# Optimization experiments

Measured on AMD Instinct MI355X. Metric: run time of the kernel, lower is better.

## Reference

```python
import jax, jax.numpy as jnp
import numpy as np

B, S, D = 2, 2048, 1024
HEADS, HEAD_DIM = 16, 64

def setup_inputs() -> dict:
    key = jax.random.key(0)
    ks = jax.random.split(key, 5)
    sc = 0.02
    return {
        "hidden_states": jax.random.normal(ks[0], (B, S, D), jnp.float32),
        "Wq": jax.random.normal(ks[1], (D, HEADS * HEAD_DIM), jnp.float32) * sc,
        "Wk": jax.random.normal(ks[2], (D, HEADS * HEAD_DIM), jnp.float32) * sc,
        "Wv": jax.random.normal(ks[3], (D, HEADS * HEAD_DIM), jnp.float32) * sc,
        "Wo": jax.random.normal(ks[4], (HEADS * HEAD_DIM, D), jnp.float32) * sc,
        "bo": jnp.zeros((D,), jnp.float32),
    }

def reference(hidden_states, Wq, Wk, Wv, Wo, bo):
    b, s, _ = hidden_states.shape
    # QKV projections (no bias, as in diffusers Attention defaults)
    q = (hidden_states @ Wq).reshape(b, s, HEADS, HEAD_DIM).transpose(0, 2, 1, 3)
    k = (hidden_states @ Wk).reshape(b, s, HEADS, HEAD_DIM).transpose(0, 2, 1, 3)
    v = (hidden_states @ Wv).reshape(b, s, HEADS, HEAD_DIM).transpose(0, 2, 1, 3)
    scale = 1.0 / jnp.sqrt(jnp.asarray(HEAD_DIM, hidden_states.dtype))
    scores = jnp.einsum('bhqd,bhkd->bhqk', q, k) * scale  # full NxN scores
    attn = jax.nn.softmax(scores, axis=-1)
    out = jnp.einsum('bhqk,bhkd->bhqd', attn, v)
    out = out.transpose(0, 2, 1, 3).reshape(b, s, HEADS * HEAD_DIM)
    return out @ Wo + bo
```

## Files before the change

kernel.cpp:

```cpp
#include <hip/hip_runtime.h>

#define B_ 2
#define S_ 2048
#define D_ 1024
#define H_ 16
#define HD_ 64
#define M_ (B_ * S_)

typedef __attribute__((ext_vector_type(4))) float f32x4;
typedef __attribute__((ext_vector_type(16))) float f32x16;
typedef __attribute__((ext_vector_type(8))) short s16x8;
typedef unsigned short u16;
typedef unsigned int u32;

#define QSCALE 0.1803368801111204f

__device__ __forceinline__ u16 f2bf(float f) {
  unsigned u = __float_as_uint(f);
  u += 0x7fffu + ((u >> 16) & 1u);
  return (u16)(u >> 16);
}

__device__ __forceinline__ u32 cvtpk_bf16(float lo, float hi) {
  u32 r;
  asm("v_cvt_pk_bf16_f32 %0, %1, %2" : "=v"(r) : "v"(lo), "v"(hi));
  return r;
}

__device__ __forceinline__ void g2lds16(const u16* g, u16* l) {
  __builtin_amdgcn_global_load_lds((const __attribute__((address_space(1))) u32*)(g),
                                   (__attribute__((address_space(3))) u32*)(l), 16, 0, 0);
}

__global__ __launch_bounds__(256) void prep_kernel(
    const float* __restrict__ X, const float* __restrict__ Wq,
    const float* __restrict__ Wk, const float* __restrict__ Wv,
    const float* __restrict__ Wo, u16* __restrict__ Xb, u16* __restrict__ Wt0) {
  __shared__ float tile[32][33];
  const int id = blockIdx.x;
  if (id < 4096) {
    int i = (id * 256 + threadIdx.x) * 4;
    const float4 v = *(const float4*)(X + i);
    ushort4 o;
    o.x = f2bf(v.x); o.y = f2bf(v.y); o.z = f2bf(v.z); o.w = f2bf(v.w);
    *(ushort4*)(Xb + i) = o;
    return;
  }
  const int id2 = id - 4096;
  const int z = id2 >> 10;
  const float* W = (z == 0) ? Wq : (z == 1) ? Wk : (z == 2) ? Wv : Wo;
  u16* Wt = Wt0 + (size_t)z * (D_ * D_);
  const float sc = (z == 0) ? QSCALE : 1.0f;
  const int tx = threadIdx.x & 31, ty = threadIdx.x >> 5;
  const int c0 = (id2 & 31) * 32, r0 = ((id2 >> 5) & 31) * 32;
#pragma unroll
  for (int j = 0; j < 32; j += 8)
    tile[ty + j][tx] = W[(size_t)(r0 + ty + j) * D_ + c0 + tx];
  __syncthreads();
#pragma unroll
  for (int j = 0; j < 32; j += 8)
    Wt[(size_t)(c0 + ty + j) * D_ + r0 + tx] = f2bf(tile[tx][ty + j] * sc);
}

__global__ __launch_bounds__(256) void gemm_qkv_kernel(
    const u16* __restrict__ Xb, const u16* __restrict__ WqT,
    const u16* __restrict__ WkT, const u16* __restrict__ WvT,
    u16* __restrict__ Qb, u16* __restrict__ Kb, u16* __restrict__ Vt) {
  __shared__ u16 As[2][128 * 32];
  __shared__ u16 Bs[2][128 * 32];
  const int tid = threadIdx.x;
  const int lane = tid & 63, wid = tid >> 6;
  const int wr = wid >> 1, wc = wid & 1;
  const int l15 = lane & 15, l4 = lane >> 4;
  const int bm = blockIdx.x * 128;
  const int bn128 = blockIdx.y;
  const int sel = bn128 >> 3;
  const u16* Wt = (sel == 0) ? WqT : (sel == 1) ? WkT : WvT;
  const int bn = (bn128 & 7) * 128;
  const int r0 = lane >> 2;
  const int c0 = lane & 3;

#define GSTAGE(buf, kt)                                                          \
  do {                                                                           \
    _Pragma("unroll") for (int j = 0; j < 2; ++j) {                              \
      const int row = (wid * 2 + j) * 16 + r0;                                   \
      g2lds16(Xb + (size_t)(bm + row) * D_ + (kt) + c0 * 8,                      \
              &As[buf][(wid * 2 + j) * 512]);                                    \
      g2lds16(Wt + (size_t)(bn + row) * D_ + (kt) + c0 * 8,                      \
              &Bs[buf][(wid * 2 + j) * 512]);                                    \
    }                                                                            \
  } while (0)

  f32x4 acc[4][4] = {};
  GSTAGE(0, 0);
  __syncthreads();
  int cur = 0;
  for (int kt = 0; kt < D_; kt += 32) {
    GSTAGE(cur ^ 1, (kt + 32) & (D_ - 1));
    s16x8 af[4], bfr[4];
#pragma unroll
    for (int i = 0; i < 4; ++i) af[i] = *(const s16x8*)&As[cur][(wr * 64 + i * 16 + l15) * 32 + l4 * 8];
#pragma unroll
    for (int j = 0; j < 4; ++j) bfr[j] = *(const s16x8*)&Bs[cur][(wc * 64 + j * 16 + l15) * 32 + l4 * 8];
#pragma unroll
    for (int i = 0; i < 4; ++i)
#pragma unroll
      for (int j = 0; j < 4; ++j)
        acc[i][j] = __builtin_amdgcn_mfma_f32_16x16x32_bf16(af[i], bfr[j], acc[i][j], 0, 0, 0);
    __syncthreads();
    cur ^= 1;
  }
#undef GSTAGE
#pragma unroll
  for (int i = 0; i < 4; ++i)
#pragma unroll
    for (int j = 0; j < 4; ++j)
#pragma unroll
      for (int r = 0; r < 4; ++r) {
        int m = bm + wr * 64 + i * 16 + l4 * 4 + r;
        int n = bn + wc * 64 + j * 16 + l15;
        int bb = m >> 11, s = m & (S_ - 1);
        int h = n >> 6, d = n & 63;
        u16 v = f2bf(acc[i][j][r]);
        size_t bhsel = (size_t)bb * H_ + h;
        if (sel == 0)      Qb[(bhsel * S_ + s) * HD_ + d] = v;
        else if (sel == 1) Kb[(bhsel * S_ + s) * HD_ + d] = v;
        else               Vt[(bhsel * HD_ + d) * S_ + s] = v;
      }
}

__global__ __launch_bounds__(512, 4) void attn_kernel(
    const u16* __restrict__ Qb, const u16* __restrict__ Kb,
    const u16* __restrict__ Vt, u16* __restrict__ Ob) {
  __shared__ char smem_raw[65536];
  typedef u16 (*lds_t)[2][4096];
  lds_t Ks = (lds_t)smem_raw;
  lds_t Vs = (lds_t)(smem_raw + 32768);
  const int tid = threadIdx.x;
  const int lane = tid & 63, wid = tid >> 6;
  const int qg = wid & 3, half = wid >> 2;
  const int l31 = lane & 31, hi = lane >> 5;
  const int id = blockIdx.x;
  const int bh = (id & 7) * 4 + ((id >> 3) >> 4);
  const int qx = (id >> 3) & 15;
  const size_t kbase = (size_t)bh * S_ * HD_;
  const size_t vbase = (size_t)bh * HD_ * S_;
  const int q0 = qx * 128 + qg * 32;
  const int r0 = lane >> 3;
  const int cs = ((lane & 7) ^ r0) * 8;
  const int kv0 = half << 10;

#define STAGE(buf, kvv)                                                          \
  do {                                                                           \
    _Pragma("unroll") for (int j = 0; j < 2; ++j) {                              \
      const int row = (qg * 2 + j) * 8 + r0;                                     \
      g2lds16(Kb + kbase + (size_t)((kvv) + row) * HD_ + cs,                     \
              &Ks[half][buf][(qg * 2 + j) * 512]);                               \
      g2lds16(Vt + vbase + (size_t)row * S_ + (kvv) + cs,                        \
              &Vs[half][buf][(qg * 2 + j) * 512]);                               \
    }                                                                            \
  } while (0)

  STAGE(0, kv0);

  s16x8 aq[4];
#pragma unroll
  for (int kc = 0; kc < 4; ++kc)
    aq[kc] = *(const s16x8*)(Qb + kbase + (size_t)(q0 + l31) * HD_ + kc * 16 + hi * 8);

  const short one_bf = (short)0x3F80;
  const s16x8 ones8 = {one_bf, one_bf, one_bf, one_bf, one_bf, one_bf, one_bf, one_bf};

  f32x16 acc0 = {}, acc1 = {}, lsacc = {};

  int choff[4];
#pragma unroll
  for (int c = 0; c < 4; ++c) choff[c] = ((c * 2 + hi) ^ (l31 & 7)) * 8;

  __syncthreads();

  for (int t = 0; t < 16; ++t) {
    const int buf = t & 1;
    STAGE(buf ^ 1, kv0 + (((t + 1) & 15) << 6));

    f32x16 s0 = {}, s1 = {};
    __builtin_amdgcn_s_setprio(1);
#pragma unroll
    for (int kc = 0; kc < 4; ++kc) {
      const s16x8 ka0 = *(const s16x8*)&Ks[half][buf][(l31) * 64 + choff[kc]];
      const s16x8 ka1 = *(const s16x8*)&Ks[half][buf][(32 + l31) * 64 + choff[kc]];
      s0 = __builtin_amdgcn_mfma_f32_32x32x16_bf16(ka0, aq[kc], s0, 0, 0, 0);
      s1 = __builtin_amdgcn_mfma_f32_32x32x16_bf16(ka1, aq[kc], s1, 0, 0, 0);
    }
    __builtin_amdgcn_s_setprio(0);

#pragma unroll
    for (int r = 0; r < 16; ++r) {
      s0[r] = __builtin_amdgcn_exp2f(s0[r]);
      s1[r] = __builtin_amdgcn_exp2f(s1[r]);
    }

    s16x8 pa[4];
#pragma unroll
    for (int c = 0; c < 4; ++c) {
      const int rr = (c & 1) * 8;
      u32 a0, a1, b0, b1;
      if (c < 2) {
        a0 = cvtpk_bf16(s0[rr + 0], s0[rr + 1]);
        a1 = cvtpk_bf16(s0[rr + 2], s0[rr + 3]);
        b0 = cvtpk_bf16(s0[rr + 4], s0[rr + 5]);
        b1 = cvtpk_bf16(s0[rr + 6], s0[rr + 7]);
      } else {
        a0 = cvtpk_bf16(s1[rr + 0], s1[rr + 1]);
        a1 = cvtpk_bf16(s1[rr + 2], s1[rr + 3]);
        b0 = cvtpk_bf16(s1[rr + 4], s1[rr + 5]);
        b1 = cvtpk_bf16(s1[rr + 6], s1[rr + 7]);
      }
      asm volatile("v_permlane32_swap_b32 %0, %1" : "+v"(a0), "+v"(b0));
      asm volatile("v_permlane32_swap_b32 %0, %1" : "+v"(a1), "+v"(b1));
      union { u32 u[4]; s16x8 v; } pk;
      pk.u[0] = a0; pk.u[1] = a1; pk.u[2] = b0; pk.u[3] = b1;
      pa[c] = pk.v;
    }

    __builtin_amdgcn_s_setprio(1);
#pragma unroll
    for (int c = 0; c < 4; ++c) {
      const s16x8 vb0 = *(const s16x8*)&Vs[half][buf][(l31) * 64 + choff[c]];
      const s16x8 vb1 = *(const s16x8*)&Vs[half][buf][(32 + l31) * 64 + choff[c]];
      acc0 = __builtin_amdgcn_mfma_f32_32x32x16_bf16(pa[c], vb0, acc0, 0, 0, 0);
      acc1 = __builtin_amdgcn_mfma_f32_32x32x16_bf16(pa[c], vb1, acc1, 0, 0, 0);
      lsacc = __builtin_amdgcn_mfma_f32_32x32x16_bf16(pa[c], ones8, lsacc, 0, 0, 0);
    }
    __builtin_amdgcn_s_setprio(0);

    __syncthreads();
  }
#undef STAGE

  float (*MB)[64][49] = (float(*)[64][49])smem_raw;
  if (half) {
#pragma unroll
    for (int r = 0; r < 16; ++r) {
      MB[qg][lane][r] = acc0[r];
      MB[qg][lane][16 + r] = acc1[r];
      MB[qg][lane][32 + r] = lsacc[r];
    }
  }
  __syncthreads();
  if (!half) {
    const int bb = bh >> 4, h = bh & 15;
#pragma unroll
    for (int r = 0; r < 16; ++r) {
      const float o0 = acc0[r] + MB[qg][lane][r];
      const float o1 = acc1[r] + MB[qg][lane][16 + r];
      const float rinv = 1.0f / (lsacc[r] + MB[qg][lane][32 + r]);
      const int qrow = (r & 3) + 8 * (r >> 2) + 4 * hi;
      const int q = q0 + qrow;
      Ob[(size_t)(bb * S_ + q) * (H_ * HD_) + h * HD_ + l31] = f2bf(o0 * rinv);
      Ob[(size_t)(bb * S_ + q) * (H_ * HD_) + h * HD_ + 32 + l31] = f2bf(o1 * rinv);
    }
  }
}

__global__ __launch_bounds__(256, 2) void gemm_o_kernel(
    const u16* __restrict__ A, const u16* __restrict__ Bt,
    const float* __restrict__ bias, float* __restrict__ C) {
  __shared__ u16 As[2][128 * 32];
  __shared__ u16 Bs[2][64 * 32];
  const int tid = threadIdx.x;
  const int lane = tid & 63, wid = tid >> 6;
  const int l15 = lane & 15, l4 = lane >> 4;
  const int bm = blockIdx.x * 128;
  const int bn = blockIdx.y * 64;
  const int r0 = lane >> 2;
  const int c0 = lane & 3;

#define GSTAGE(buf, kt)                                                          \
  do {                                                                           \
    _Pragma("unroll") for (int j = 0; j < 2; ++j) {                              \
      const int row = (wid * 2 + j) * 16 + r0;                                   \
      g2lds16(A + (size_t)(bm + row) * D_ + (kt) + c0 * 8,                       \
              &As[buf][(wid * 2 + j) * 512]);                                    \
    }                                                                            \
    g2lds16(Bt + (size_t)(bn + wid * 16 + r0) * D_ + (kt) + c0 * 8,              \
            &Bs[buf][wid * 512]);                                                \
  } while (0)

  f32x4 acc[2][4] = {};
  GSTAGE(0, 0);
  __syncthreads();
  int cur = 0;
  for (int kt = 0; kt < D_; kt += 32) {
    GSTAGE(cur ^ 1, (kt + 32) & (D_ - 1));
    s16x8 af[2], bfr[4];
#pragma unroll
    for (int i = 0; i < 2; ++i) af[i] = *(const s16x8*)&As[cur][(wid * 32 + i * 16 + l15) * 32 + l4 * 8];
#pragma unroll
    for (int j = 0; j < 4; ++j) bfr[j] = *(const s16x8*)&Bs[cur][(j * 16 + l15) * 32 + l4 * 8];
#pragma unroll
    for (int i = 0; i < 2; ++i)
#pragma unroll
      for (int j = 0; j < 4; ++j)
        acc[i][j] = __builtin_amdgcn_mfma_f32_16x16x32_bf16(af[i], bfr[j], acc[i][j], 0, 0, 0);
    __syncthreads();
    cur ^= 1;
  }
#undef GSTAGE
#pragma unroll
  for (int i = 0; i < 2; ++i)
#pragma unroll
    for (int j = 0; j < 4; ++j)
#pragma unroll
      for (int r = 0; r < 4; ++r) {
        int m = bm + wid * 32 + i * 16 + l4 * 4 + r;
        int n = bn + j * 16 + l15;
        C[(size_t)m * D_ + n] = acc[i][j][r] + bias[n];
      }
}

extern "C" void kernel_launch(void* const* d_in, const int* in_sizes, int n_in,
                              void* d_out, int out_size, void* d_ws, size_t ws_size,
                              hipStream_t stream) {
  const float* X  = (const float*)d_in[0];
  const float* Wq = (const float*)d_in[1];
  const float* Wk = (const float*)d_in[2];
  const float* Wv = (const float*)d_in[3];
  const float* Wo = (const float*)d_in[4];
  const float* bo = (const float*)d_in[5];
  float* out = (float*)d_out;

  char* w = (char*)d_ws;
  u16* Xb  = (u16*)(w);
  u16* WT  = (u16*)(w + (8u << 20));
  u16* WqT = WT;
  u16* WkT = WT + (1u << 20);
  u16* WvT = WT + (2u << 20);
  u16* WoT = WT + (3u << 20);
  u16* Qb  = (u16*)(w + (16u << 20));
  u16* Kb  = (u16*)(w + (24u << 20));
  u16* Vt  = (u16*)(w + (32u << 20));
  u16* Ob  = (u16*)(w + (40u << 20));

  prep_kernel<<<8192, 256, 0, stream>>>(X, Wq, Wk, Wv, Wo, Xb, WT);
  gemm_qkv_kernel<<<dim3(32, 24), 256, 0, stream>>>(Xb, WqT, WkT, WvT, Qb, Kb, Vt);
  attn_kernel<<<512, 512, 0, stream>>>(Qb, Kb, Vt, Ob);
  gemm_o_kernel<<<dim3(32, 16), 256, 0, stream>>>(Ob, WoT, bo, out);
}
```

Baseline: 115.6 us.

## Process two 32-row query tiles per wave and compute row sums with VALU

Each wave now handles 64 query rows (two 32-row tiles) against the same K/V tile loaded into LDS, halving the grid to 256 blocks and reusing each K/V LDS fragment for two MFMAs. The ones-vector MFMA used to compute softmax row sums is replaced by per-lane VALU accumulation of exp values, followed by cross-lane shuffles at the end. This removes a third of the PV MFMAs and halves K/V staging traffic per query row. The cost is higher register pressure (launch bounds relaxed to 2 waves-occupancy hint) and only 256 blocks, which may leave CUs underfilled on a 256-CU part.

```diff
diff --git a/kernel.cpp b/kernel.cpp
--- a/kernel.cpp
+++ b/kernel.cpp
@@ -129,7 +129,7 @@
       }
 }
 
-__global__ __launch_bounds__(512, 4) void attn_kernel(
+__global__ __launch_bounds__(512, 2) void attn_kernel(
     const u16* __restrict__ Qb, const u16* __restrict__ Kb,
     const u16* __restrict__ Vt, u16* __restrict__ Ob) {
   __shared__ char smem_raw[65536];
@@ -141,11 +141,11 @@
   const int qg = wid & 3, half = wid >> 2;
   const int l31 = lane & 31, hi = lane >> 5;
   const int id = blockIdx.x;
-  const int bh = (id & 7) * 4 + ((id >> 3) >> 4);
-  const int qx = (id >> 3) & 15;
+  const int bh = (id & 7) * 4 + (id >> 6);
+  const int qx = (id >> 3) & 7;
   const size_t kbase = (size_t)bh * S_ * HD_;
   const size_t vbase = (size_t)bh * HD_ * S_;
-  const int q0 = qx * 128 + qg * 32;
+  const int q0 = qx * 256 + qg * 64;
   const int r0 = lane >> 3;
   const int cs = ((lane & 7) ^ r0) * 8;
   const int kv0 = half << 10;
@@ -163,15 +163,15 @@
 
   STAGE(0, kv0);
 
-  s16x8 aq[4];
-#pragma unroll
-  for (int kc = 0; kc < 4; ++kc)
-    aq[kc] = *(const s16x8*)(Qb + kbase + (size_t)(q0 + l31) * HD_ + kc * 16 + hi * 8);
-
-  const short one_bf = (short)0x3F80;
-  const s16x8 ones8 = {one_bf, one_bf, one_bf, one_bf, one_bf, one_bf, one_bf, one_bf};
-
-  f32x16 acc0 = {}, acc1 = {}, lsacc = {};
+  s16x8 aqA[4], aqB[4];
+#pragma unroll
+  for (int kc = 0; kc < 4; ++kc) {
+    aqA[kc] = *(const s16x8*)(Qb + kbase + (size_t)(q0 + l31) * HD_ + kc * 16 + hi * 8);
+    aqB[kc] = *(const s16x8*)(Qb + kbase + (size_t)(q0 + 32 + l31) * HD_ + kc * 16 + hi * 8);
+  }
+
+  f32x16 accA0 = {}, accA1 = {}, accB0 = {}, accB1 = {};
+  float lsA = 0.f, lsB = 0.f;
 
   int choff[4];
 #pragma unroll
@@ -183,44 +183,74 @@
     const int buf = t & 1;
     STAGE(buf ^ 1, kv0 + (((t + 1) & 15) << 6));
 
-    f32x16 s0 = {}, s1 = {};
+    f32x16 sA0 = {}, sA1 = {}, sB0 = {}, sB1 = {};
     __builtin_amdgcn_s_setprio(1);
 #pragma unroll
     for (int kc = 0; kc < 4; ++kc) {
       const s16x8 ka0 = *(const s16x8*)&Ks[half][buf][(l31) * 64 + choff[kc]];
       const s16x8 ka1 = *(const s16x8*)&Ks[half][buf][(32 + l31) * 64 + choff[kc]];
-      s0 = __builtin_amdgcn_mfma_f32_32x32x16_bf16(ka0, aq[kc], s0, 0, 0, 0);
-      s1 = __builtin_amdgcn_mfma_f32_32x32x16_bf16(ka1, aq[kc], s1, 0, 0, 0);
+      sA0 = __builtin_amdgcn_mfma_f32_32x32x16_bf16(ka0, aqA[kc], sA0, 0, 0, 0);
+      sB0 = __builtin_amdgcn_mfma_f32_32x32x16_bf16(ka0, aqB[kc], sB0, 0, 0, 0);
+      sA1 = __builtin_amdgcn_mfma_f32_32x32x16_bf16(ka1, aqA[kc], sA1, 0, 0, 0);
+      sB1 = __builtin_amdgcn_mfma_f32_32x32x16_bf16(ka1, aqB[kc], sB1, 0, 0, 0);
     }
     __builtin_amdgcn_s_setprio(0);
 
-#pragma unroll
-    for (int r = 0; r < 16; ++r) {
-      s0[r] = __builtin_amdgcn_exp2f(s0[r]);
-      s1[r] = __builtin_amdgcn_exp2f(s1[r]);
-    }
-
-    s16x8 pa[4];
+    float tA = 0.f, tB = 0.f;
+#pragma unroll
+    for (int r = 0; r < 16; ++r) {
+      sA0[r] = __builtin_amdgcn_exp2f(sA0[r]);
+      sA1[r] = __builtin_amdgcn_exp2f(sA1[r]);
+      sB0[r] = __builtin_amdgcn_exp2f(sB0[r]);
+      sB1[r] = __builtin_amdgcn_exp2f(sB1[r]);
+      tA += sA0[r] + sA1[r];
+      tB += sB0[r] + sB1[r];
+    }
+    lsA += tA;
+    lsB += tB;
+
+    s16x8 paA[4], paB[4];
 #pragma unroll
     for (int c = 0; c < 4; ++c) {
       const int rr = (c & 1) * 8;
       u32 a0, a1, b0, b1;
       if (c < 2) {
-        a0 = cvtpk_bf16(s0[rr + 0], s0[rr + 1]);
-        a1 = cvtpk_bf16(s0[rr + 2], s0[rr + 3]);
-        b0 = cvtpk_bf16(s0[rr + 4], s0[rr + 5]);
-        b1 = cvtpk_bf16(s0[rr + 6], s0[rr + 7]);
+        a0 = cvtpk_bf16(sA0[rr + 0], sA0[rr + 1]);
+        a1 = cvtpk_bf16(sA0[rr + 2], sA0[rr + 3]);
+        b0 = cvtpk_bf16(sA0[rr + 4], sA0[rr + 5]);
+        b1 = cvtpk_bf16(sA0[rr + 6], sA0[rr + 7]);
       } else {
-        a0 = cvtpk_bf16(s1[rr + 0], s1[rr + 1]);
-        a1 = cvtpk_bf16(s1[rr + 2], s1[rr + 3]);
-        b0 = cvtpk_bf16(s1[rr + 4], s1[rr + 5]);
-        b1 = cvtpk_bf16(s1[rr + 6], s1[rr + 7]);
+        a0 = cvtpk_bf16(sA1[rr + 0], sA1[rr + 1]);
+        a1 = cvtpk_bf16(sA1[rr + 2], sA1[rr + 3]);
+        b0 = cvtpk_bf16(sA1[rr + 4], sA1[rr + 5]);
+        b1 = cvtpk_bf16(sA1[rr + 6], sA1[rr + 7]);
       }
       asm volatile("v_permlane32_swap_b32 %0, %1" : "+v"(a0), "+v"(b0));
       asm volatile("v_permlane32_swap_b32 %0, %1" : "+v"(a1), "+v"(b1));
       union { u32 u[4]; s16x8 v; } pk;
       pk.u[0] = a0; pk.u[1] = a1; pk.u[2] = b0; pk.u[3] = b1;
-      pa[c] = pk.v;
+      paA[c] = pk.v;
+    }
+#pragma unroll
+    for (int c = 0; c < 4; ++c) {
+      const int rr = (c & 1) * 8;
+      u32 a0, a1, b0, b1;
+      if (c < 2) {
+        a0 = cvtpk_bf16(sB0[rr + 0], sB0[rr + 1]);
+        a1 = cvtpk_bf16(sB0[rr + 2], sB0[rr + 3]);
+        b0 = cvtpk_bf16(sB0[rr + 4], sB0[rr + 5]);
+        b1 = cvtpk_bf16(sB0[rr + 6], sB0[rr + 7]);
+      } else {
+        a0 = cvtpk_bf16(sB1[rr + 0], sB1[rr + 1]);
+        a1 = cvtpk_bf16(sB1[rr + 2], sB1[rr + 3]);
+        b0 = cvtpk_bf16(sB1[rr + 4], sB1[rr + 5]);
+        b1 = cvtpk_bf16(sB1[rr + 6], sB1[rr + 7]);
+      }
+      asm volatile("v_permlane32_swap_b32 %0, %1" : "+v"(a0), "+v"(b0));
+      asm volatile("v_permlane32_swap_b32 %0, %1" : "+v"(a1), "+v"(b1));
+      union { u32 u[4]; s16x8 v; } pk;
+      pk.u[0] = a0; pk.u[1] = a1; pk.u[2] = b0; pk.u[3] = b1;
+      paB[c] = pk.v;
     }
 
     __builtin_amdgcn_s_setprio(1);
@@ -228,9 +258,10 @@
     for (int c = 0; c < 4; ++c) {
       const s16x8 vb0 = *(const s16x8*)&Vs[half][buf][(l31) * 64 + choff[c]];
       const s16x8 vb1 = *(const s16x8*)&Vs[half][buf][(32 + l31) * 64 + choff[c]];
-      acc0 = __builtin_amdgcn_mfma_f32_32x32x16_bf16(pa[c], vb0, acc0, 0, 0, 0);
-      acc1 = __builtin_amdgcn_mfma_f32_32x32x16_bf16(pa[c], vb1, acc1, 0, 0, 0);
-      lsacc = __builtin_amdgcn_mfma_f32_32x32x16_bf16(pa[c], ones8, lsacc, 0, 0, 0);
+      accA0 = __builtin_amdgcn_mfma_f32_32x32x16_bf16(paA[c], vb0, accA0, 0, 0, 0);
+      accB0 = __builtin_amdgcn_mfma_f32_32x32x16_bf16(paB[c], vb0, accB0, 0, 0, 0);
+      accA1 = __builtin_amdgcn_mfma_f32_32x32x16_bf16(paA[c], vb1, accA1, 0, 0, 0);
+      accB1 = __builtin_amdgcn_mfma_f32_32x32x16_bf16(paB[c], vb1, accB1, 0, 0, 0);
     }
     __builtin_amdgcn_s_setprio(0);
 
@@ -238,27 +269,60 @@
   }
 #undef STAGE
 
-  float (*MB)[64][49] = (float(*)[64][49])smem_raw;
+  lsA += __shfl_xor(lsA, 32);
+  lsB += __shfl_xor(lsB, 32);
+  const int bb = bh >> 4, h = bh & 15;
+  float (*MB)[64][33] = (float(*)[64][33])smem_raw;
+
   if (half) {
 #pragma unroll
     for (int r = 0; r < 16; ++r) {
-      MB[qg][lane][r] = acc0[r];
-      MB[qg][lane][16 + r] = acc1[r];
-      MB[qg][lane][32 + r] = lsacc[r];
-    }
+      MB[qg][lane][r] = accA0[r];
+      MB[qg][lane][16 + r] = accA1[r];
+    }
+    MB[qg][lane][32] = lsA;
   }
   __syncthreads();
   if (!half) {
-    const int bb = bh >> 4, h = bh & 15;
-#pragma unroll
-    for (int r = 0; r < 16; ++r) {
-      const float o0 = acc0[r] + MB[qg][lane][r];
-      const float o1 = acc1[r] + MB[qg][lane][16 + r];
-      const float rinv = 1.0f / (lsacc[r] + MB[qg][lane][32 + r]);
+    lsA += MB[qg][lane][32];
+#pragma unroll
+    for (int r = 0; r < 16; ++r) {
+      accA0[r] += MB[qg][lane][r];
+      accA1[r] += MB[qg][lane][16 + r];
+    }
+#pragma unroll
+    for (int r = 0; r < 16; ++r) {
       const int qrow = (r & 3) + 8 * (r >> 2) + 4 * hi;
+      const float rinv = 1.0f / __shfl(lsA, qrow);
       const int q = q0 + qrow;
-      Ob[(size_t)(bb * S_ + q) * (H_ * HD_) + h * HD_ + l31] = f2bf(o0 * rinv);
-      Ob[(size_t)(bb * S_ + q) * (H_ * HD_) + h * HD_ + 32 + l31] = f2bf(o1 * rinv);
+      Ob[(size_t)(bb * S_ + q) * (H_ * HD_) + h * HD_ + l31] = f2bf(accA0[r] * rinv);
+      Ob[(size_t)(bb * S_ + q) * (H_ * HD_) + h * HD_ + 32 + l31] = f2bf(accA1[r] * rinv);
+    }
+  }
+  __syncthreads();
+  if (half) {
+#pragma unroll
+    for (int r = 0; r < 16; ++r) {
+      MB[qg][lane][r] = accB0[r];
+      MB[qg][lane][16 + r] = accB1[r];
+    }
+    MB[qg][lane][32] = lsB;
+  }
+  __syncthreads();
+  if (!half) {
+    lsB += MB[qg][lane][32];
+#pragma unroll
+    for (int r = 0; r < 16; ++r) {
+      accB0[r] += MB[qg][lane][r];
+      accB1[r] += MB[qg][lane][16 + r];
+    }
+#pragma unroll
+    for (int r = 0; r < 16; ++r) {
+      const int qrow = (r & 3) + 8 * (r >> 2) + 4 * hi;
+      const float rinv = 1.0f / __shfl(lsB, qrow);
+      const int q = q0 + 32 + qrow;
+      Ob[(size_t)(bb * S_ + q) * (H_ * HD_) + h * HD_ + l31] = f2bf(accB0[r] * rinv);
+      Ob[(size_t)(bb * S_ + q) * (H_ * HD_) + h * HD_ + 32 + l31] = f2bf(accB1[r] * rinv);
     }
   }
 }
@@ -344,6 +408,6 @@
 
   prep_kernel<<<8192, 256, 0, stream>>>(X, Wq, Wk, Wv, Wo, Xb, WT);
   gemm_qkv_kernel<<<dim3(32, 24), 256, 0, stream>>>(Xb, WqT, WkT, WvT, Qb, Kb, Vt);
-  attn_kernel<<<512, 512, 0, stream>>>(Qb, Kb, Vt, Ob);
+  attn_kernel<<<256, 512, 0, stream>>>(Qb, Kb, Vt, Ob);
   gemm_o_kernel<<<dim3(32, 16), 256, 0, stream>>>(Ob, WoT, bo, out);
 }
```

New measurement: 113.8 us. Within noise of the previous version (-1.6%).

## Drop KV split in attention; use triple-buffered LDS with partial vmcnt waits

Applied to the files above, without the earlier changes.

The attention kernel no longer splits the KV range across two half-blocks of 4 waves. Each 256-thread block now walks all 32 KV tiles itself, which removes the LDS reduction and extra barrier in the epilogue. K/V staging moves to a 3-deep ring buffer with two tiles prefetched. Each iteration waits with a partial vmcnt instead of a full syncthreads, so loads can overlap more compute. The cost is half as many waves per block and a longer serial loop per wave, which may lower latency hiding and occupancy.

```diff
diff --git a/kernel.cpp b/kernel.cpp
--- a/kernel.cpp
+++ b/kernel.cpp
@@ -129,45 +129,42 @@
       }
 }
 
-__global__ __launch_bounds__(512, 4) void attn_kernel(
+__global__ __launch_bounds__(256, 2) void attn_kernel(
     const u16* __restrict__ Qb, const u16* __restrict__ Kb,
     const u16* __restrict__ Vt, u16* __restrict__ Ob) {
-  __shared__ char smem_raw[65536];
-  typedef u16 (*lds_t)[2][4096];
-  lds_t Ks = (lds_t)smem_raw;
-  lds_t Vs = (lds_t)(smem_raw + 32768);
+  __shared__ u16 Ks[3][4096];
+  __shared__ u16 Vs[3][4096];
   const int tid = threadIdx.x;
   const int lane = tid & 63, wid = tid >> 6;
-  const int qg = wid & 3, half = wid >> 2;
   const int l31 = lane & 31, hi = lane >> 5;
   const int id = blockIdx.x;
   const int bh = (id & 7) * 4 + ((id >> 3) >> 4);
   const int qx = (id >> 3) & 15;
   const size_t kbase = (size_t)bh * S_ * HD_;
   const size_t vbase = (size_t)bh * HD_ * S_;
-  const int q0 = qx * 128 + qg * 32;
+  const int q0 = qx * 128 + wid * 32;
   const int r0 = lane >> 3;
   const int cs = ((lane & 7) ^ r0) * 8;
-  const int kv0 = half << 10;
-
-#define STAGE(buf, kvv)                                                          \
+
+#define STAGE(b, kvv)                                                            \
   do {                                                                           \
     _Pragma("unroll") for (int j = 0; j < 2; ++j) {                              \
-      const int row = (qg * 2 + j) * 8 + r0;                                     \
+      const int row = (wid * 2 + j) * 8 + r0;                                    \
       g2lds16(Kb + kbase + (size_t)((kvv) + row) * HD_ + cs,                     \
-              &Ks[half][buf][(qg * 2 + j) * 512]);                               \
+              &Ks[b][(wid * 2 + j) * 512]);                                      \
       g2lds16(Vt + vbase + (size_t)row * S_ + (kvv) + cs,                        \
-              &Vs[half][buf][(qg * 2 + j) * 512]);                               \
+              &Vs[b][(wid * 2 + j) * 512]);                                      \
     }                                                                            \
   } while (0)
 
-  STAGE(0, kv0);
-
   s16x8 aq[4];
 #pragma unroll
   for (int kc = 0; kc < 4; ++kc)
     aq[kc] = *(const s16x8*)(Qb + kbase + (size_t)(q0 + l31) * HD_ + kc * 16 + hi * 8);
 
+  STAGE(0, 0);
+  STAGE(1, 64);
+
   const short one_bf = (short)0x3F80;
   const s16x8 ones8 = {one_bf, one_bf, one_bf, one_bf, one_bf, one_bf, one_bf, one_bf};
 
@@ -177,18 +174,21 @@
 #pragma unroll
   for (int c = 0; c < 4; ++c) choff[c] = ((c * 2 + hi) ^ (l31 & 7)) * 8;
 
-  __syncthreads();
-
-  for (int t = 0; t < 16; ++t) {
-    const int buf = t & 1;
-    STAGE(buf ^ 1, kv0 + (((t + 1) & 15) << 6));
+  asm volatile("s_waitcnt vmcnt(4)" ::: "memory");
+  __builtin_amdgcn_s_barrier();
+  __builtin_amdgcn_sched_barrier(0);
+
+  int b0 = 0, b1 = 1, b2 = 2;
+#pragma unroll 1
+  for (int t = 0; t < 32; ++t) {
+    STAGE(b2, ((t + 2) & 31) << 6);
 
     f32x16 s0 = {}, s1 = {};
     __builtin_amdgcn_s_setprio(1);
 #pragma unroll
     for (int kc = 0; kc < 4; ++kc) {
-      const s16x8 ka0 = *(const s16x8*)&Ks[half][buf][(l31) * 64 + choff[kc]];
-      const s16x8 ka1 = *(const s16x8*)&Ks[half][buf][(32 + l31) * 64 + choff[kc]];
+      const s16x8 ka0 = *(const s16x8*)&Ks[b0][(l31) * 64 + choff[kc]];
+      const s16x8 ka1 = *(const s16x8*)&Ks[b0][(32 + l31) * 64 + choff[kc]];
       s0 = __builtin_amdgcn_mfma_f32_32x32x16_bf16(ka0, aq[kc], s0, 0, 0, 0);
       s1 = __builtin_amdgcn_mfma_f32_32x32x16_bf16(ka1, aq[kc], s1, 0, 0, 0);
     }
@@ -204,62 +204,52 @@
 #pragma unroll
     for (int c = 0; c < 4; ++c) {
       const int rr = (c & 1) * 8;
-      u32 a0, a1, b0, b1;
+      u32 a0, a1, b0_, b1_;
       if (c < 2) {
         a0 = cvtpk_bf16(s0[rr + 0], s0[rr + 1]);
         a1 = cvtpk_bf16(s0[rr + 2], s0[rr + 3]);
-        b0 = cvtpk_bf16(s0[rr + 4], s0[rr + 5]);
-        b1 = cvtpk_bf16(s0[rr + 6], s0[rr + 7]);
+        b0_ = cvtpk_bf16(s0[rr + 4], s0[rr + 5]);
+        b1_ = cvtpk_bf16(s0[rr + 6], s0[rr + 7]);
       } else {
         a0 = cvtpk_bf16(s1[rr + 0], s1[rr + 1]);
         a1 = cvtpk_bf16(s1[rr + 2], s1[rr + 3]);
-        b0 = cvtpk_bf16(s1[rr + 4], s1[rr + 5]);
-        b1 = cvtpk_bf16(s1[rr + 6], s1[rr + 7]);
+        b0_ = cvtpk_bf16(s1[rr + 4], s1[rr + 5]);
+        b1_ = cvtpk_bf16(s1[rr + 6], s1[rr + 7]);
       }
-      asm volatile("v_permlane32_swap_b32 %0, %1" : "+v"(a0), "+v"(b0));
-      asm volatile("v_permlane32_swap_b32 %0, %1" : "+v"(a1), "+v"(b1));
+      asm volatile("v_permlane32_swap_b32 %0, %1" : "+v"(a0), "+v"(b0_));
+      asm volatile("v_permlane32_swap_b32 %0, %1" : "+v"(a1), "+v"(b1_));
       union { u32 u[4]; s16x8 v; } pk;
-      pk.u[0] = a0; pk.u[1] = a1; pk.u[2] = b0; pk.u[3] = b1;
+      pk.u[0] = a0; pk.u[1] = a1; pk.u[2] = b0_; pk.u[3] = b1_;
       pa[c] = pk.v;
     }
 
     __builtin_amdgcn_s_setprio(1);
 #pragma unroll
     for (int c = 0; c < 4; ++c) {
-      const s16x8 vb0 = *(const s16x8*)&Vs[half][buf][(l31) * 64 + choff[c]];
-      const s16x8 vb1 = *(const s16x8*)&Vs[half][buf][(32 + l31) * 64 + choff[c]];
+      const s16x8 vb0 = *(const s16x8*)&Vs[b0][(l31) * 64 + choff[c]];
+      const s16x8 vb1 = *(const s16x8*)&Vs[b0][(32 + l31) * 64 + choff[c]];
       acc0 = __builtin_amdgcn_mfma_f32_32x32x16_bf16(pa[c], vb0, acc0, 0, 0, 0);
       acc1 = __builtin_amdgcn_mfma_f32_32x32x16_bf16(pa[c], vb1, acc1, 0, 0, 0);
       lsacc = __builtin_amdgcn_mfma_f32_32x32x16_bf16(pa[c], ones8, lsacc, 0, 0, 0);
     }
     __builtin_amdgcn_s_setprio(0);
 
-    __syncthreads();
+    asm volatile("s_waitcnt vmcnt(4)" ::: "memory");
+    __builtin_amdgcn_s_barrier();
+    __builtin_amdgcn_sched_barrier(0);
+
+    const int tmp = b0; b0 = b1; b1 = b2; b2 = tmp;
   }
 #undef STAGE
 
-  float (*MB)[64][49] = (float(*)[64][49])smem_raw;
-  if (half) {
-#pragma unroll
-    for (int r = 0; r < 16; ++r) {
-      MB[qg][lane][r] = acc0[r];
-      MB[qg][lane][16 + r] = acc1[r];
-      MB[qg][lane][32 + r] = lsacc[r];
-    }
-  }
-  __syncthreads();
-  if (!half) {
-    const int bb = bh >> 4, h = bh & 15;
-#pragma unroll
-    for (int r = 0; r < 16; ++r) {
-      const float o0 = acc0[r] + MB[qg][lane][r];
-      const float o1 = acc1[r] + MB[qg][lane][16 + r];
-      const float rinv = 1.0f / (lsacc[r] + MB[qg][lane][32 + r]);
-      const int qrow = (r & 3) + 8 * (r >> 2) + 4 * hi;
-      const int q = q0 + qrow;
-      Ob[(size_t)(bb * S_ + q) * (H_ * HD_) + h * HD_ + l31] = f2bf(o0 * rinv);
-      Ob[(size_t)(bb * S_ + q) * (H_ * HD_) + h * HD_ + 32 + l31] = f2bf(o1 * rinv);
-    }
+  const int bb = bh >> 4, h = bh & 15;
+#pragma unroll
+  for (int r = 0; r < 16; ++r) {
+    const float rinv = 1.0f / lsacc[r];
+    const int qrow = (r & 3) + 8 * (r >> 2) + 4 * hi;
+    const int q = q0 + qrow;
+    Ob[(size_t)(bb * S_ + q) * (H_ * HD_) + h * HD_ + l31] = f2bf(acc0[r] * rinv);
+    Ob[(size_t)(bb * S_ + q) * (H_ * HD_) + h * HD_ + 32 + l31] = f2bf(acc1[r] * rinv);
   }
 }
 
@@ -344,6 +334,6 @@
 
   prep_kernel<<<8192, 256, 0, stream>>>(X, Wq, Wk, Wv, Wo, Xb, WT);
   gemm_qkv_kernel<<<dim3(32, 24), 256, 0, stream>>>(Xb, WqT, WkT, WvT, Qb, Kb, Vt);
-  attn_kernel<<<512, 512, 0, stream>>>(Qb, Kb, Vt, Ob);
+  attn_kernel<<<512, 256, 0, stream>>>(Qb, Kb, Vt, Ob);
   gemm_o_kernel<<<dim3(32, 16), 256, 0, stream>>>(Ob, WoT, bo, out);
 }
```

New measurement: 118.1 us. 1.02x slower.
